# Kernel tuning notes

Measured on AMD Instinct MI355X. Metric: run time of the kernel, lower is better.

Reference implementation:

```python
import jax, jax.numpy as jnp
import numpy as np

B, S, HID = 2, 2048, 4096
H, KH, D = 32, 8, 128
WINDOW = 1024
THETA = 1000000.0


def setup_inputs() -> dict:
    key = jax.random.key(0)
    ks = jax.random.split(key, 5)
    scale = 0.02
    hidden_states = jax.random.normal(ks[0], (B, S, HID), dtype=jnp.float32)
    wq = jax.random.normal(ks[1], (HID, H * D), dtype=jnp.float32) * scale
    wk = jax.random.normal(ks[2], (HID, KH * D), dtype=jnp.float32) * scale
    wv = jax.random.normal(ks[3], (HID, KH * D), dtype=jnp.float32) * scale
    wo = jax.random.normal(ks[4], (H * D, HID), dtype=jnp.float32) * scale
    position_ids = jnp.broadcast_to(jnp.arange(S, dtype=jnp.int64 if jax.config.jax_enable_x64 else jnp.int32), (B, S))
    return {"hidden_states": hidden_states, "position_ids": position_ids,
            "wq": wq, "wk": wk, "wv": wv, "wo": wo}


def _rope_sin_cos(position_ids):
    # inv_freq over even dims, emb = concat(freqs, freqs) -> [b, s, D]
    inv_freq = 1.0 / (THETA ** (jnp.arange(0, D, 2, dtype=jnp.float32) / D))
    angles = position_ids.astype(jnp.float32)[..., None] * inv_freq  # [b, s, D/2]
    emb = jnp.concatenate([angles, angles], axis=-1)  # [b, s, D]
    return jnp.sin(emb)[:, None, :, :], jnp.cos(emb)[:, None, :, :]  # [b,1,s,D]


def _rotate_half(x):
    x1, x2 = jnp.split(x, 2, axis=-1)
    return jnp.concatenate([-x2, x1], axis=-1)


def _apply_rope(x, sin, cos):
    return x * cos + _rotate_half(x) * sin


def reference(hidden_states, position_ids, wq, wk, wv, wo):
    b, s, _ = hidden_states.shape
    # projections -> [b, heads, s, d]
    q = (hidden_states @ wq).reshape(b, s, H, D).transpose(0, 2, 1, 3)
    k = (hidden_states @ wk).reshape(b, s, KH, D).transpose(0, 2, 1, 3)
    v = (hidden_states @ wv).reshape(b, s, KH, D).transpose(0, 2, 1, 3)
    sin, cos = _rope_sin_cos(position_ids)
    q = _apply_rope(q, sin, cos)
    k = _apply_rope(k, sin, cos)
    # repeat kv heads for GQA: [b, KH, s, d] -> [b, H, s, d]
    rep = H // KH
    k = jnp.repeat(k, rep, axis=1)
    v = jnp.repeat(v, rep, axis=1)
    # sliding-window causal mask
    i = jnp.arange(s)[:, None]
    j = jnp.arange(s)[None, :]
    mask = (j <= i) & (i - j < WINDOW)  # [s, s]
    scores = jnp.einsum("bhqd,bhkd->bhqk", q, k) / jnp.sqrt(jnp.asarray(D, q.dtype))
    neg = jnp.finfo(scores.dtype).min
    scores = jnp.where(mask[None, None, :, :], scores, neg)
    attn = jax.nn.softmax(scores, axis=-1)
    out = jnp.einsum("bhqk,bhkd->bhqd", attn, v)
    out = out.transpose(0, 2, 1, 3).reshape(b, s, H * D)
    return out @ wo
```

## Files before the change

kernel.cpp:

```cpp
#include <hip/hip_runtime.h>
#include <hip/hip_bf16.h>
#include <math.h>

typedef __attribute__((ext_vector_type(8))) __bf16 bf16x8;
typedef __attribute__((ext_vector_type(4))) float f32x4;

#define MFMA16(a, b, c) __builtin_amdgcn_mfma_f32_16x16x32_bf16((a), (b), (c), 0, 0, 0)

__device__ inline void gld_lds16(const __hip_bfloat16* g, __hip_bfloat16* l) {
    __builtin_amdgcn_global_load_lds(
        (const __attribute__((address_space(1))) void*)g,
        (__attribute__((address_space(3))) void*)l, 16, 0, 0);
}

#define RAW_BARRIER() __builtin_amdgcn_s_barrier()
#define WAIT_LGKM0()                                          \
    do {                                                      \
        asm volatile("s_waitcnt lgkmcnt(0)" ::: "memory");    \
        __builtin_amdgcn_sched_barrier(0);                    \
    } while (0)
#define WAIT_VM(N) asm volatile("s_waitcnt vmcnt(" #N ")" ::: "memory")

__global__ void cast_bf16_kernel(const float* __restrict__ in, __hip_bfloat16* __restrict__ out) {
    int i = (blockIdx.x * blockDim.x + threadIdx.x) * 4;
    float4 v = *(const float4*)(in + i);
    out[i + 0] = __float2bfloat16(v.x);
    out[i + 1] = __float2bfloat16(v.y);
    out[i + 2] = __float2bfloat16(v.z);
    out[i + 3] = __float2bfloat16(v.w);
}

__global__ void transpose_cast_kernel(const float* __restrict__ w, __hip_bfloat16* __restrict__ wt,
                                      int K, int N) {
    __shared__ float tile[32][33];
    int n0 = blockIdx.x * 32, k0 = blockIdx.y * 32;
    int tx = threadIdx.x;
    int ty = threadIdx.y;
#pragma unroll
    for (int r = 0; r < 4; r++) {
        int k = k0 + ty + r * 8;
        tile[ty + r * 8][tx] = w[(size_t)k * N + n0 + tx];
    }
    __syncthreads();
#pragma unroll
    for (int r = 0; r < 4; r++) {
        int n = n0 + ty + r * 8;
        wt[(size_t)n * K + k0 + tx] = __float2bfloat16(tile[tx][ty + r * 8]);
    }
}

constexpr int TILE = 256 * 64;

template <typename EPILOGUE>
__device__ __forceinline__ void gemm256_8phase(
    const __hip_bfloat16* __restrict__ A, const __hip_bfloat16* __restrict__ Bt,
    int m0, int n0, int K, __hip_bfloat16* As, __hip_bfloat16* Bs, EPILOGUE epi) {
    int tid = threadIdx.x;
    int wave = tid >> 6, lane = tid & 63;
    int l15 = lane & 15, quad = lane >> 4;
    int wr = wave >> 2, wc = wave & 3;

    int lr = lane >> 3;
    int c8 = (lane & 7) ^ lr;
    const __hip_bfloat16* aG = A + (size_t)(m0 + wave * 8 + lr) * K + c8 * 8;
    const __hip_bfloat16* bG = Bt + (size_t)(n0 + wave * 8 + lr) * K + c8 * 8;
    int stRow = wave * 8;

    int e3 = l15 & 7;
    int s0 = (quad ^ e3) * 8;
    int s1 = ((4 + quad) ^ e3) * 8;

    f32x4 acc[8][4];
#pragma unroll
    for (int mi = 0; mi < 8; mi++)
#pragma unroll
        for (int ni = 0; ni < 4; ni++) acc[mi][ni] = (f32x4){0.f, 0.f, 0.f, 0.f};

    const int NT = K >> 6;

    auto stA = [&](int buf, int kt, int i) {
        gld_lds16(aG + (size_t)kt * 64 + (size_t)(i * 64) * K,
                  As + buf * TILE + (stRow + i * 64) * 64);
    };
    auto stB = [&](int buf, int kt, int i) {
        gld_lds16(bG + (size_t)kt * 64 + (size_t)(i * 64) * K,
                  Bs + buf * TILE + (stRow + i * 64) * 64);
    };

#pragma unroll
    for (int i = 0; i < 4; i++) stA(0, 0, i);
#pragma unroll
    for (int i = 0; i < 4; i++) stB(0, 0, i);
    {
        int k1 = (1 < NT) ? 1 : 0;
#pragma unroll
        for (int i = 0; i < 4; i++) stA(1, k1, i);
    }
    WAIT_VM(4);
    RAW_BARRIER();

    int cur = 0;
    for (int t = 0; t < NT; ++t) {
        int ktB = (t + 1 < NT) ? t + 1 : NT - 1;
        int ktA = (t + 2 < NT) ? t + 2 : NT - 1;
        const __hip_bfloat16* af = As + cur * TILE + (wr * 128 + l15) * 64;
        const __hip_bfloat16* bf = Bs + cur * TILE + (wc * 64 + l15) * 64;
        bf16x8 a0[4][2], a1[4][2], b0[2][2], b1[2][2];

#pragma unroll
        for (int mi = 0; mi < 4; mi++) {
            a0[mi][0] = *(const bf16x8*)(af + mi * 1024 + s0);
            a0[mi][1] = *(const bf16x8*)(af + mi * 1024 + s1);
        }
#pragma unroll
        for (int ni = 0; ni < 2; ni++) {
            b0[ni][0] = *(const bf16x8*)(bf + ni * 1024 + s0);
            b0[ni][1] = *(const bf16x8*)(bf + ni * 1024 + s1);
        }
        stB(cur ^ 1, ktB, 0);
        stB(cur ^ 1, ktB, 1);
        RAW_BARRIER();
        WAIT_LGKM0();
        __builtin_amdgcn_s_setprio(1);
#pragma unroll
        for (int mi = 0; mi < 4; mi++)
#pragma unroll
            for (int ni = 0; ni < 2; ni++) {
                acc[mi][ni] = MFMA16(a0[mi][0], b0[ni][0], acc[mi][ni]);
                acc[mi][ni] = MFMA16(a0[mi][1], b0[ni][1], acc[mi][ni]);
            }
        __builtin_amdgcn_s_setprio(0);
        RAW_BARRIER();

#pragma unroll
        for (int mi = 0; mi < 4; mi++) {
            a1[mi][0] = *(const bf16x8*)(af + (mi + 4) * 1024 + s0);
            a1[mi][1] = *(const bf16x8*)(af + (mi + 4) * 1024 + s1);
        }
        stB(cur ^ 1, ktB, 2);
        stB(cur ^ 1, ktB, 3);
        RAW_BARRIER();
        WAIT_LGKM0();
        __builtin_amdgcn_s_setprio(1);
#pragma unroll
        for (int mi = 0; mi < 4; mi++)
#pragma unroll
            for (int ni = 0; ni < 2; ni++) {
                acc[mi + 4][ni] = MFMA16(a1[mi][0], b0[ni][0], acc[mi + 4][ni]);
                acc[mi + 4][ni] = MFMA16(a1[mi][1], b0[ni][1], acc[mi + 4][ni]);
            }
        __builtin_amdgcn_s_setprio(0);
        RAW_BARRIER();

#pragma unroll
        for (int ni = 0; ni < 2; ni++) {
            b1[ni][0] = *(const bf16x8*)(bf + (ni + 2) * 1024 + s0);
            b1[ni][1] = *(const bf16x8*)(bf + (ni + 2) * 1024 + s1);
        }
        stA(cur, ktA, 0);
        stA(cur, ktA, 1);
        RAW_BARRIER();
        WAIT_LGKM0();
        __builtin_amdgcn_s_setprio(1);
#pragma unroll
        for (int mi = 0; mi < 4; mi++)
#pragma unroll
            for (int ni = 0; ni < 2; ni++) {
                acc[mi][ni + 2] = MFMA16(a0[mi][0], b1[ni][0], acc[mi][ni + 2]);
                acc[mi][ni + 2] = MFMA16(a0[mi][1], b1[ni][1], acc[mi][ni + 2]);
            }
        __builtin_amdgcn_s_setprio(0);
        RAW_BARRIER();

        stA(cur, ktA, 2);
        stA(cur, ktA, 3);
        RAW_BARRIER();
        __builtin_amdgcn_s_setprio(1);
#pragma unroll
        for (int mi = 0; mi < 4; mi++)
#pragma unroll
            for (int ni = 0; ni < 2; ni++) {
                acc[mi + 4][ni + 2] = MFMA16(a1[mi][0], b1[ni][0], acc[mi + 4][ni + 2]);
                acc[mi + 4][ni + 2] = MFMA16(a1[mi][1], b1[ni][1], acc[mi + 4][ni + 2]);
            }
        __builtin_amdgcn_s_setprio(0);
        WAIT_VM(4);
        RAW_BARRIER();
        cur ^= 1;
    }
    WAIT_VM(0);
    epi(acc, wr, wc, l15, quad);
}

__global__ __launch_bounds__(512, 2) void gemm_qkv_kernel(
    const __hip_bfloat16* __restrict__ Xb,
    const __hip_bfloat16* __restrict__ Wt,
    __hip_bfloat16* __restrict__ Qraw,
    __hip_bfloat16* __restrict__ Kraw,
    __hip_bfloat16* __restrict__ Vtt) {
    __shared__ __hip_bfloat16 As[2 * TILE];
    __shared__ __hip_bfloat16 Bs[2 * TILE];
    int m0 = blockIdx.y * 256, n0 = blockIdx.x * 256;
    gemm256_8phase(Xb, Wt, m0, n0, 4096, As, Bs,
        [&](f32x4 (&acc)[8][4], int wr, int wc, int l15, int quad) {
#pragma unroll
            for (int mi = 0; mi < 8; mi++) {
#pragma unroll
                for (int ni = 0; ni < 4; ni++) {
                    int n = n0 + wc * 64 + ni * 16 + l15;
#pragma unroll
                    for (int r = 0; r < 4; r++) {
                        int m = m0 + wr * 128 + mi * 16 + quad * 4 + r;
                        int bb = m >> 11, s = m & 2047;
                        __hip_bfloat16 hv = __float2bfloat16(acc[mi][ni][r]);
                        if (n < 4096) {
                            int hh = n >> 7, d = n & 127;
                            Qraw[(((size_t)(bb * 32 + hh)) * 2048 + s) * 128 + d] = hv;
                        } else if (n < 5120) {
                            int n2 = n - 4096, hh = n2 >> 7, d = n2 & 127;
                            Kraw[(((size_t)(bb * 8 + hh)) * 2048 + s) * 128 + d] = hv;
                        } else {
                            int n2 = n - 5120, hh = n2 >> 7, d = n2 & 127;
                            Vtt[((((size_t)(bb * 8 + hh)) * 32 + (s >> 6)) * 128 + d) * 64 + (s & 63)] = hv;
                        }
                    }
                }
            }
        });
}

__global__ __launch_bounds__(512, 2) void gemm_out_kernel(
    const __hip_bfloat16* __restrict__ A, const __hip_bfloat16* __restrict__ Bt,
    float* __restrict__ C) {
    __shared__ __hip_bfloat16 As[2 * TILE];
    __shared__ __hip_bfloat16 Bs[2 * TILE];
    int m0 = blockIdx.y * 256, n0 = blockIdx.x * 256;
    gemm256_8phase(A, Bt, m0, n0, 4096, As, Bs,
        [&](f32x4 (&acc)[8][4], int wr, int wc, int l15, int quad) {
            const int N = 4096;
#pragma unroll
            for (int mi = 0; mi < 8; mi++) {
#pragma unroll
                for (int ni = 0; ni < 4; ni++) {
                    int n = n0 + wc * 64 + ni * 16 + l15;
#pragma unroll
                    for (int r = 0; r < 4; r++) {
                        int m = m0 + wr * 128 + mi * 16 + quad * 4 + r;
                        C[(size_t)m * N + n] = acc[mi][ni][r];
                    }
                }
            }
        });
}

__global__ void rope_kernel(__hip_bfloat16* __restrict__ x, const int* __restrict__ pos_ids,
                            int nheads) {
    int idx = blockIdx.x * blockDim.x + threadIdx.x;
    int d = idx & 63;
    int s = (idx >> 6) & 2047;
    int bh = idx >> 17;
    int b = bh / nheads;
    float p = (float)pos_ids[b * 2048 + s];
    float inv = exp2f(-(float)d * 0.31143075889f);
    float ang = p * inv;
    float sn, cs;
    __sincosf(ang, &sn, &cs);
    size_t base = ((size_t)bh * 2048 + s) * 128;
    float x1 = __bfloat162float(x[base + d]);
    float x2 = __bfloat162float(x[base + d + 64]);
    x[base + d]      = __float2bfloat16(x1 * cs - x2 * sn);
    x[base + d + 64] = __float2bfloat16(x2 * cs + x1 * sn);
}

__global__ __launch_bounds__(256) void attn_kernel(
    const __hip_bfloat16* __restrict__ Qb, const __hip_bfloat16* __restrict__ Kb,
    const __hip_bfloat16* __restrict__ Vtt, __hip_bfloat16* __restrict__ AO) {
    const int S = 2048, D = 128;
    __shared__ __hip_bfloat16 Ks[64 * 128];
    __shared__ __hip_bfloat16 Vs[128 * 64];
    __shared__ __hip_bfloat16 Pl[4][16][72];

    int tid = threadIdx.x;
    int wave = tid >> 6, lane = tid & 63;
    int l15 = lane & 15, quad = lane >> 4;
    int base = blockIdx.x * 64;
    int i0 = base + wave * 16;
    int h = blockIdx.y, b = blockIdx.z;
    int kh = h >> 2;
    const __hip_bfloat16* Qh = Qb + (size_t)(b * 32 + h) * S * D;
    const __hip_bfloat16* Kh = Kb + (size_t)(b * 8 + kh) * S * D;
    const __hip_bfloat16* Vh = Vtt + (size_t)(b * 8 + kh) * S * D;

    bf16x8 qf[4];
    {
        const __hip_bfloat16* qrow = Qh + (size_t)(i0 + l15) * D + quad * 8;
#pragma unroll
        for (int kk = 0; kk < 4; kk++) qf[kk] = *(const bf16x8*)(qrow + kk * 32);
    }
    f32x4 o[8];
#pragma unroll
    for (int f = 0; f < 8; f++) o[f] = (f32x4){0.f, 0.f, 0.f, 0.f};
    float lrow[4] = {0.f, 0.f, 0.f, 0.f};

    int kst = (base > 1023) ? ((base - 1023) & ~63) : 0;
    const float c2 = 0.12751878882f;
    int e3 = l15 & 7;

    for (int key0 = kst; key0 <= base; key0 += 64) {
#pragma unroll
        for (int i = 0; i < 4; i++) {
            int rb = wave * 16 + i * 4;
            int row = rb + (lane >> 4);
            int c = (lane & 15) ^ (row & 7);
            gld_lds16(Kh + (size_t)(key0 + row) * 128 + c * 8, Ks + rb * 128);
        }
        const __hip_bfloat16* Vtile = Vh + (size_t)(key0 >> 6) * (128 * 64);
#pragma unroll
        for (int i = 0; i < 4; i++) {
            int db = wave * 32 + i * 8;
            int row = db + (lane >> 3);
            int c = (lane & 7) ^ (row & 7);
            gld_lds16(Vtile + (size_t)row * 64 + c * 8, Vs + db * 64);
        }
        __syncthreads();

        bool alive = (key0 <= i0 + 15) && (key0 + 63 >= i0 - 1023);
        if (alive) {
            f32x4 sc[4];
#pragma unroll
            for (int kb = 0; kb < 4; kb++) {
                sc[kb] = (f32x4){0.f, 0.f, 0.f, 0.f};
                const __hip_bfloat16* krow = Ks + (kb * 16 + l15) * 128;
#pragma unroll
                for (int kk = 0; kk < 4; kk++) {
                    int slot = ((kk << 2) | quad) ^ e3;
                    bf16x8 kf = *(const bf16x8*)(krow + slot * 8);
                    sc[kb] = MFMA16(qf[kk], kf, sc[kb]);
                }
            }
            bool interior = (key0 + 63 <= i0) && (key0 >= i0 - 1008);
            if (interior) {
#pragma unroll
                for (int kb = 0; kb < 4; kb++)
#pragma unroll
                    for (int r = 0; r < 4; r++) {
                        float p = __builtin_amdgcn_exp2f(sc[kb][r] * c2);
                        lrow[r] += p;
                        Pl[wave][quad * 4 + r][kb * 16 + l15] = __float2bfloat16(p);
                    }
            } else {
#pragma unroll
                for (int kb = 0; kb < 4; kb++)
#pragma unroll
                    for (int r = 0; r < 4; r++) {
                        int i = i0 + quad * 4 + r;
                        int j = key0 + kb * 16 + l15;
                        float v = (j <= i && i - j < 1024) ? sc[kb][r] * c2 : -1e30f;
                        float p = __builtin_amdgcn_exp2f(v);
                        lrow[r] += p;
                        Pl[wave][quad * 4 + r][kb * 16 + l15] = __float2bfloat16(p);
                    }
            }
            bf16x8 pf0 = *(const bf16x8*)(&Pl[wave][l15][quad * 8]);
            bf16x8 pf1 = *(const bf16x8*)(&Pl[wave][l15][32 + quad * 8]);
            int s0 = quad ^ e3, s1 = (4 + quad) ^ e3;
#pragma unroll
            for (int f = 0; f < 8; f++) {
                const __hip_bfloat16* vrow = Vs + (f * 16 + l15) * 64;
                bf16x8 v0 = *(const bf16x8*)(vrow + s0 * 8);
                bf16x8 v1 = *(const bf16x8*)(vrow + s1 * 8);
                o[f] = MFMA16(pf0, v0, o[f]);
                o[f] = MFMA16(pf1, v1, o[f]);
            }
        }
        __syncthreads();
    }

#pragma unroll
    for (int r = 0; r < 4; r++) {
#pragma unroll
        for (int msk = 1; msk < 16; msk <<= 1) lrow[r] += __shfl_xor(lrow[r], msk, 64);
    }
#pragma unroll
    for (int r = 0; r < 4; r++) {
        int srow = i0 + quad * 4 + r;
        float invl = 1.f / lrow[r];
        __hip_bfloat16* orow = AO + ((size_t)(b * 2048 + srow) * 4096) + h * 128;
#pragma unroll
        for (int f = 0; f < 8; f++) orow[f * 16 + l15] = __float2bfloat16(o[f][r] * invl);
    }
}

extern "C" void kernel_launch(void* const* d_in, const int* in_sizes, int n_in,
                              void* d_out, int out_size, void* d_ws, size_t ws_size,
                              hipStream_t stream) {
    (void)in_sizes; (void)n_in; (void)out_size;
    const float* hidden = (const float*)d_in[0];
    const int* pos = (const int*)d_in[1];
    const float* wq = (const float*)d_in[2];
    const float* wk = (const float*)d_in[3];
    const float* wv = (const float*)d_in[4];
    const float* wo = (const float*)d_in[5];
    float* out = (float*)d_out;

    const int M = 4096;
    char* ws = (char*)d_ws;
    size_t off = 0;
    auto alloc = [&](size_t bytes) { char* p = ws + off; off += bytes; return p; };
    __hip_bfloat16* Xb    = (__hip_bfloat16*)alloc((size_t)M * 4096 * 2);
    __hip_bfloat16* Wqkvt = (__hip_bfloat16*)alloc((size_t)6144 * 4096 * 2);
    __hip_bfloat16* Wot   = (__hip_bfloat16*)alloc((size_t)4096 * 4096 * 2);
    __hip_bfloat16* Qb    = (__hip_bfloat16*)alloc((size_t)M * 4096 * 2);
    __hip_bfloat16* Kb    = (__hip_bfloat16*)alloc((size_t)M * 1024 * 2);
    __hip_bfloat16* Vtt   = (__hip_bfloat16*)alloc((size_t)M * 1024 * 2);
    __hip_bfloat16* AO    = (__hip_bfloat16*)alloc((size_t)M * 4096 * 2);
    if (off > ws_size) return;

    cast_bf16_kernel<<<(M * 4096) / 1024, 256, 0, stream>>>(hidden, Xb);
    dim3 tb(32, 8);
    transpose_cast_kernel<<<dim3(128, 128), tb, 0, stream>>>(wq, Wqkvt, 4096, 4096);
    transpose_cast_kernel<<<dim3(32, 128),  tb, 0, stream>>>(wk, Wqkvt + (size_t)4096 * 4096, 4096, 1024);
    transpose_cast_kernel<<<dim3(32, 128),  tb, 0, stream>>>(wv, Wqkvt + (size_t)5120 * 4096, 4096, 1024);
    transpose_cast_kernel<<<dim3(128, 128), tb, 0, stream>>>(wo, Wot, 4096, 4096);

    gemm_qkv_kernel<<<dim3(24, 16), 512, 0, stream>>>(Xb, Wqkvt, Qb, Kb, Vtt);

    rope_kernel<<<(2 * 32 * 2048 * 64) / 256, 256, 0, stream>>>(Qb, pos, 32);
    rope_kernel<<<(2 * 8 * 2048 * 64) / 256, 256, 0, stream>>>(Kb, pos, 8);

    attn_kernel<<<dim3(32, 32, 2), 256, 0, stream>>>(Qb, Kb, Vtt, AO);

    gemm_out_kernel<<<dim3(16, 16), 512, 0, stream>>>(AO, Wot, out);
}
```

Before: 841.6 us.

## Double-buffer attention K/V tiles and use smaller-tile QKV GEMM

```diff
diff --git a/kernel.cpp b/kernel.cpp
--- a/kernel.cpp
+++ b/kernel.cpp
@@ -49,168 +49,83 @@
     }
 }
 
-constexpr int TILE = 256 * 64;
-
 template <typename EPILOGUE>
-__device__ __forceinline__ void gemm256_8phase(
+__device__ __forceinline__ void gemm128_bk64(
     const __hip_bfloat16* __restrict__ A, const __hip_bfloat16* __restrict__ Bt,
     int m0, int n0, int K, __hip_bfloat16* As, __hip_bfloat16* Bs, EPILOGUE epi) {
     int tid = threadIdx.x;
     int wave = tid >> 6, lane = tid & 63;
     int l15 = lane & 15, quad = lane >> 4;
-    int wr = wave >> 2, wc = wave & 3;
 
     int lr = lane >> 3;
     int c8 = (lane & 7) ^ lr;
     const __hip_bfloat16* aG = A + (size_t)(m0 + wave * 8 + lr) * K + c8 * 8;
     const __hip_bfloat16* bG = Bt + (size_t)(n0 + wave * 8 + lr) * K + c8 * 8;
-    int stRow = wave * 8;
-
+    __hip_bfloat16* aL = As + wave * 512;
+    __hip_bfloat16* bL = Bs + wave * 512;
+
+    int wm = wave & 1, wn = wave >> 1;
     int e3 = l15 & 7;
     int s0 = (quad ^ e3) * 8;
     int s1 = ((4 + quad) ^ e3) * 8;
-
-    f32x4 acc[8][4];
-#pragma unroll
-    for (int mi = 0; mi < 8; mi++)
+    const __hip_bfloat16* afr = As + (wm * 64 + l15) * 64;
+    const __hip_bfloat16* bfr = Bs + (wn * 64 + l15) * 64;
+
+    f32x4 acc[4][4];
+#pragma unroll
+    for (int mi = 0; mi < 4; mi++)
 #pragma unroll
         for (int ni = 0; ni < 4; ni++) acc[mi][ni] = (f32x4){0.f, 0.f, 0.f, 0.f};
 
-    const int NT = K >> 6;
-
-    auto stA = [&](int buf, int kt, int i) {
-        gld_lds16(aG + (size_t)kt * 64 + (size_t)(i * 64) * K,
-                  As + buf * TILE + (stRow + i * 64) * 64);
-    };
-    auto stB = [&](int buf, int kt, int i) {
-        gld_lds16(bG + (size_t)kt * 64 + (size_t)(i * 64) * K,
-                  Bs + buf * TILE + (stRow + i * 64) * 64);
-    };
-
-#pragma unroll
-    for (int i = 0; i < 4; i++) stA(0, 0, i);
-#pragma unroll
-    for (int i = 0; i < 4; i++) stB(0, 0, i);
-    {
-        int k1 = (1 < NT) ? 1 : 0;
-#pragma unroll
-        for (int i = 0; i < 4; i++) stA(1, k1, i);
-    }
-    WAIT_VM(4);
-    RAW_BARRIER();
-
-    int cur = 0;
-    for (int t = 0; t < NT; ++t) {
-        int ktB = (t + 1 < NT) ? t + 1 : NT - 1;
-        int ktA = (t + 2 < NT) ? t + 2 : NT - 1;
-        const __hip_bfloat16* af = As + cur * TILE + (wr * 128 + l15) * 64;
-        const __hip_bfloat16* bf = Bs + cur * TILE + (wc * 64 + l15) * 64;
-        bf16x8 a0[4][2], a1[4][2], b0[2][2], b1[2][2];
-
+    for (int k0 = 0; k0 < K; k0 += 64) {
+#pragma unroll
+        for (int i = 0; i < 4; i++) {
+            gld_lds16(aG + k0 + (size_t)(i * 32) * K, aL + i * 2048);
+            gld_lds16(bG + k0 + (size_t)(i * 32) * K, bL + i * 2048);
+        }
+        __syncthreads();
+        bf16x8 a0[4], b0[4], a1[4], b1[4];
 #pragma unroll
         for (int mi = 0; mi < 4; mi++) {
-            a0[mi][0] = *(const bf16x8*)(af + mi * 1024 + s0);
-            a0[mi][1] = *(const bf16x8*)(af + mi * 1024 + s1);
-        }
-#pragma unroll
-        for (int ni = 0; ni < 2; ni++) {
-            b0[ni][0] = *(const bf16x8*)(bf + ni * 1024 + s0);
-            b0[ni][1] = *(const bf16x8*)(bf + ni * 1024 + s1);
-        }
-        stB(cur ^ 1, ktB, 0);
-        stB(cur ^ 1, ktB, 1);
-        RAW_BARRIER();
-        WAIT_LGKM0();
-        __builtin_amdgcn_s_setprio(1);
+            a0[mi] = *(const bf16x8*)(afr + mi * 1024 + s0);
+            a1[mi] = *(const bf16x8*)(afr + mi * 1024 + s1);
+        }
+#pragma unroll
+        for (int ni = 0; ni < 4; ni++) {
+            b0[ni] = *(const bf16x8*)(bfr + ni * 1024 + s0);
+            b1[ni] = *(const bf16x8*)(bfr + ni * 1024 + s1);
+        }
 #pragma unroll
         for (int mi = 0; mi < 4; mi++)
 #pragma unroll
-            for (int ni = 0; ni < 2; ni++) {
-                acc[mi][ni] = MFMA16(a0[mi][0], b0[ni][0], acc[mi][ni]);
-                acc[mi][ni] = MFMA16(a0[mi][1], b0[ni][1], acc[mi][ni]);
-            }
-        __builtin_amdgcn_s_setprio(0);
-        RAW_BARRIER();
-
-#pragma unroll
-        for (int mi = 0; mi < 4; mi++) {
-            a1[mi][0] = *(const bf16x8*)(af + (mi + 4) * 1024 + s0);
-            a1[mi][1] = *(const bf16x8*)(af + (mi + 4) * 1024 + s1);
-        }
-        stB(cur ^ 1, ktB, 2);
-        stB(cur ^ 1, ktB, 3);
-        RAW_BARRIER();
-        WAIT_LGKM0();
-        __builtin_amdgcn_s_setprio(1);
-#pragma unroll
-        for (int mi = 0; mi < 4; mi++)
-#pragma unroll
-            for (int ni = 0; ni < 2; ni++) {
-                acc[mi + 4][ni] = MFMA16(a1[mi][0], b0[ni][0], acc[mi + 4][ni]);
-                acc[mi + 4][ni] = MFMA16(a1[mi][1], b0[ni][1], acc[mi + 4][ni]);
-            }
-        __builtin_amdgcn_s_setprio(0);
-        RAW_BARRIER();
-
-#pragma unroll
-        for (int ni = 0; ni < 2; ni++) {
-            b1[ni][0] = *(const bf16x8*)(bf + (ni + 2) * 1024 + s0);
-            b1[ni][1] = *(const bf16x8*)(bf + (ni + 2) * 1024 + s1);
-        }
-        stA(cur, ktA, 0);
-        stA(cur, ktA, 1);
-        RAW_BARRIER();
-        WAIT_LGKM0();
-        __builtin_amdgcn_s_setprio(1);
-#pragma unroll
-        for (int mi = 0; mi < 4; mi++)
-#pragma unroll
-            for (int ni = 0; ni < 2; ni++) {
-                acc[mi][ni + 2] = MFMA16(a0[mi][0], b1[ni][0], acc[mi][ni + 2]);
-                acc[mi][ni + 2] = MFMA16(a0[mi][1], b1[ni][1], acc[mi][ni + 2]);
-            }
-        __builtin_amdgcn_s_setprio(0);
-        RAW_BARRIER();
-
-        stA(cur, ktA, 2);
-        stA(cur, ktA, 3);
-        RAW_BARRIER();
-        __builtin_amdgcn_s_setprio(1);
-#pragma unroll
-        for (int mi = 0; mi < 4; mi++)
-#pragma unroll
-            for (int ni = 0; ni < 2; ni++) {
-                acc[mi + 4][ni + 2] = MFMA16(a1[mi][0], b1[ni][0], acc[mi + 4][ni + 2]);
-                acc[mi + 4][ni + 2] = MFMA16(a1[mi][1], b1[ni][1], acc[mi + 4][ni + 2]);
-            }
-        __builtin_amdgcn_s_setprio(0);
-        WAIT_VM(4);
-        RAW_BARRIER();
-        cur ^= 1;
-    }
-    WAIT_VM(0);
-    epi(acc, wr, wc, l15, quad);
-}
-
-__global__ __launch_bounds__(512, 2) void gemm_qkv_kernel(
+            for (int ni = 0; ni < 4; ni++) {
+                acc[mi][ni] = MFMA16(a0[mi], b0[ni], acc[mi][ni]);
+                acc[mi][ni] = MFMA16(a1[mi], b1[ni], acc[mi][ni]);
+            }
+        __syncthreads();
+    }
+    epi(acc, wm, wn, l15, quad);
+}
+
+__global__ __launch_bounds__(256) void gemm_qkv_kernel(
     const __hip_bfloat16* __restrict__ Xb,
     const __hip_bfloat16* __restrict__ Wt,
     __hip_bfloat16* __restrict__ Qraw,
     __hip_bfloat16* __restrict__ Kraw,
     __hip_bfloat16* __restrict__ Vtt) {
-    __shared__ __hip_bfloat16 As[2 * TILE];
-    __shared__ __hip_bfloat16 Bs[2 * TILE];
-    int m0 = blockIdx.y * 256, n0 = blockIdx.x * 256;
-    gemm256_8phase(Xb, Wt, m0, n0, 4096, As, Bs,
-        [&](f32x4 (&acc)[8][4], int wr, int wc, int l15, int quad) {
-#pragma unroll
-            for (int mi = 0; mi < 8; mi++) {
+    __shared__ __hip_bfloat16 As[128 * 64];
+    __shared__ __hip_bfloat16 Bs[128 * 64];
+    int m0 = blockIdx.y * 128, n0 = blockIdx.x * 128;
+    gemm128_bk64(Xb, Wt, m0, n0, 4096, As, Bs,
+        [&](f32x4 (&acc)[4][4], int wm, int wn, int l15, int quad) {
+#pragma unroll
+            for (int mi = 0; mi < 4; mi++) {
 #pragma unroll
                 for (int ni = 0; ni < 4; ni++) {
-                    int n = n0 + wc * 64 + ni * 16 + l15;
+                    int n = n0 + wn * 64 + ni * 16 + l15;
 #pragma unroll
                     for (int r = 0; r < 4; r++) {
-                        int m = m0 + wr * 128 + mi * 16 + quad * 4 + r;
+                        int m = m0 + wm * 64 + mi * 16 + quad * 4 + r;
                         int bb = m >> 11, s = m & 2047;
                         __hip_bfloat16 hv = __float2bfloat16(acc[mi][ni][r]);
                         if (n < 4096) {
@@ -227,6 +142,149 @@
                 }
             }
         });
+}
+
+constexpr int TILE = 256 * 64;
+
+template <typename EPILOGUE>
+__device__ __forceinline__ void gemm256_8phase(
+    const __hip_bfloat16* __restrict__ A, const __hip_bfloat16* __restrict__ Bt,
+    int m0, int n0, int K, __hip_bfloat16* As, __hip_bfloat16* Bs, EPILOGUE epi) {
+    int tid = threadIdx.x;
+    int wave = tid >> 6, lane = tid & 63;
+    int l15 = lane & 15, quad = lane >> 4;
+    int wr = wave >> 2, wc = wave & 3;
+
+    int lr = lane >> 3;
+    int c8 = (lane & 7) ^ lr;
+    const __hip_bfloat16* aG = A + (size_t)(m0 + wave * 8 + lr) * K + c8 * 8;
+    const __hip_bfloat16* bG = Bt + (size_t)(n0 + wave * 8 + lr) * K + c8 * 8;
+    int stRow = wave * 8;
+
+    int e3 = l15 & 7;
+    int s0 = (quad ^ e3) * 8;
+    int s1 = ((4 + quad) ^ e3) * 8;
+
+    f32x4 acc[8][4];
+#pragma unroll
+    for (int mi = 0; mi < 8; mi++)
+#pragma unroll
+        for (int ni = 0; ni < 4; ni++) acc[mi][ni] = (f32x4){0.f, 0.f, 0.f, 0.f};
+
+    const int NT = K >> 6;
+
+    auto stA = [&](int buf, int kt, int i) {
+        gld_lds16(aG + (size_t)kt * 64 + (size_t)(i * 64) * K,
+                  As + buf * TILE + (stRow + i * 64) * 64);
+    };
+    auto stB = [&](int buf, int kt, int i) {
+        gld_lds16(bG + (size_t)kt * 64 + (size_t)(i * 64) * K,
+                  Bs + buf * TILE + (stRow + i * 64) * 64);
+    };
+
+#pragma unroll
+    for (int i = 0; i < 4; i++) stA(0, 0, i);
+#pragma unroll
+    for (int i = 0; i < 4; i++) stB(0, 0, i);
+    {
+        int k1 = (1 < NT) ? 1 : 0;
+#pragma unroll
+        for (int i = 0; i < 4; i++) stA(1, k1, i);
+    }
+    WAIT_VM(4);
+    RAW_BARRIER();
+
+    int cur = 0;
+    for (int t = 0; t < NT; ++t) {
+        int ktB = (t + 1 < NT) ? t + 1 : NT - 1;
+        int ktA = (t + 2 < NT) ? t + 2 : NT - 1;
+        const __hip_bfloat16* af = As + cur * TILE + (wr * 128 + l15) * 64;
+        const __hip_bfloat16* bf = Bs + cur * TILE + (wc * 64 + l15) * 64;
+        bf16x8 a0[4][2], a1[4][2], b0[2][2], b1[2][2];
+
+#pragma unroll
+        for (int mi = 0; mi < 4; mi++) {
+            a0[mi][0] = *(const bf16x8*)(af + mi * 1024 + s0);
+            a0[mi][1] = *(const bf16x8*)(af + mi * 1024 + s1);
+        }
+#pragma unroll
+        for (int ni = 0; ni < 2; ni++) {
+            b0[ni][0] = *(const bf16x8*)(bf + ni * 1024 + s0);
+            b0[ni][1] = *(const bf16x8*)(bf + ni * 1024 + s1);
+        }
+        stB(cur ^ 1, ktB, 0);
+        stB(cur ^ 1, ktB, 1);
+        RAW_BARRIER();
+        WAIT_LGKM0();
+        __builtin_amdgcn_s_setprio(1);
+#pragma unroll
+        for (int mi = 0; mi < 4; mi++)
+#pragma unroll
+            for (int ni = 0; ni < 2; ni++) {
+                acc[mi][ni] = MFMA16(a0[mi][0], b0[ni][0], acc[mi][ni]);
+                acc[mi][ni] = MFMA16(a0[mi][1], b0[ni][1], acc[mi][ni]);
+            }
+        __builtin_amdgcn_s_setprio(0);
+        RAW_BARRIER();
+
+#pragma unroll
+        for (int mi = 0; mi < 4; mi++) {
+            a1[mi][0] = *(const bf16x8*)(af + (mi + 4) * 1024 + s0);
+            a1[mi][1] = *(const bf16x8*)(af + (mi + 4) * 1024 + s1);
+        }
+        stB(cur ^ 1, ktB, 2);
+        stB(cur ^ 1, ktB, 3);
+        RAW_BARRIER();
+        WAIT_LGKM0();
+        __builtin_amdgcn_s_setprio(1);
+#pragma unroll
+        for (int mi = 0; mi < 4; mi++)
+#pragma unroll
+            for (int ni = 0; ni < 2; ni++) {
+                acc[mi + 4][ni] = MFMA16(a1[mi][0], b0[ni][0], acc[mi + 4][ni]);
+                acc[mi + 4][ni] = MFMA16(a1[mi][1], b0[ni][1], acc[mi + 4][ni]);
+            }
+        __builtin_amdgcn_s_setprio(0);
+        RAW_BARRIER();
+
+#pragma unroll
+        for (int ni = 0; ni < 2; ni++) {
+            b1[ni][0] = *(const bf16x8*)(bf + (ni + 2) * 1024 + s0);
+            b1[ni][1] = *(const bf16x8*)(bf + (ni + 2) * 1024 + s1);
+        }
+        stA(cur, ktA, 0);
+        stA(cur, ktA, 1);
+        RAW_BARRIER();
+        WAIT_LGKM0();
+        __builtin_amdgcn_s_setprio(1);
+#pragma unroll
+        for (int mi = 0; mi < 4; mi++)
+#pragma unroll
+            for (int ni = 0; ni < 2; ni++) {
+                acc[mi][ni + 2] = MFMA16(a0[mi][0], b1[ni][0], acc[mi][ni + 2]);
+                acc[mi][ni + 2] = MFMA16(a0[mi][1], b1[ni][1], acc[mi][ni + 2]);
+            }
+        __builtin_amdgcn_s_setprio(0);
+        RAW_BARRIER();
+
+        stA(cur, ktA, 2);
+        stA(cur, ktA, 3);
+        RAW_BARRIER();
+        __builtin_amdgcn_s_setprio(1);
+#pragma unroll
+        for (int mi = 0; mi < 4; mi++)
+#pragma unroll
+            for (int ni = 0; ni < 2; ni++) {
+                acc[mi + 4][ni + 2] = MFMA16(a1[mi][0], b1[ni][0], acc[mi + 4][ni + 2]);
+                acc[mi + 4][ni + 2] = MFMA16(a1[mi][1], b1[ni][1], acc[mi + 4][ni + 2]);
+            }
+        __builtin_amdgcn_s_setprio(0);
+        WAIT_VM(4);
+        RAW_BARRIER();
+        cur ^= 1;
+    }
+    WAIT_VM(0);
+    epi(acc, wr, wc, l15, quad);
 }
 
 __global__ __launch_bounds__(512, 2) void gemm_out_kernel(
@@ -276,8 +334,8 @@
     const __hip_bfloat16* __restrict__ Qb, const __hip_bfloat16* __restrict__ Kb,
     const __hip_bfloat16* __restrict__ Vtt, __hip_bfloat16* __restrict__ AO) {
     const int S = 2048, D = 128;
-    __shared__ __hip_bfloat16 Ks[64 * 128];
-    __shared__ __hip_bfloat16 Vs[128 * 64];
+    __shared__ __hip_bfloat16 Ks[2][64 * 128];
+    __shared__ __hip_bfloat16 Vs[2][128 * 64];
     __shared__ __hip_bfloat16 Pl[4][16][72];
 
     int tid = threadIdx.x;
@@ -306,13 +364,13 @@
     const float c2 = 0.12751878882f;
     int e3 = l15 & 7;
 
-    for (int key0 = kst; key0 <= base; key0 += 64) {
+    auto stage = [&](int key0, int buf) {
 #pragma unroll
         for (int i = 0; i < 4; i++) {
             int rb = wave * 16 + i * 4;
             int row = rb + (lane >> 4);
             int c = (lane & 15) ^ (row & 7);
-            gld_lds16(Kh + (size_t)(key0 + row) * 128 + c * 8, Ks + rb * 128);
+            gld_lds16(Kh + (size_t)(key0 + row) * 128 + c * 8, &Ks[buf][rb * 128]);
         }
         const __hip_bfloat16* Vtile = Vh + (size_t)(key0 >> 6) * (128 * 64);
 #pragma unroll
@@ -320,17 +378,30 @@
             int db = wave * 32 + i * 8;
             int row = db + (lane >> 3);
             int c = (lane & 7) ^ (row & 7);
-            gld_lds16(Vtile + (size_t)row * 64 + c * 8, Vs + db * 64);
-        }
-        __syncthreads();
+            gld_lds16(Vtile + (size_t)row * 64 + c * 8, &Vs[buf][db * 64]);
+        }
+    };
+
+    stage(kst, 0);
+
+    for (int key0 = kst; key0 <= base; key0 += 64) {
+        int buf = ((key0 - kst) >> 6) & 1;
+        if (key0 + 64 <= base) {
+            stage(key0 + 64, buf ^ 1);
+            WAIT_VM(8);
+        } else {
+            WAIT_VM(0);
+        }
+        RAW_BARRIER();
 
         bool alive = (key0 <= i0 + 15) && (key0 + 63 >= i0 - 1023);
         if (alive) {
             f32x4 sc[4];
+            __builtin_amdgcn_s_setprio(1);
 #pragma unroll
             for (int kb = 0; kb < 4; kb++) {
                 sc[kb] = (f32x4){0.f, 0.f, 0.f, 0.f};
-                const __hip_bfloat16* krow = Ks + (kb * 16 + l15) * 128;
+                const __hip_bfloat16* krow = &Ks[buf][(kb * 16 + l15) * 128];
 #pragma unroll
                 for (int kk = 0; kk < 4; kk++) {
                     int slot = ((kk << 2) | quad) ^ e3;
@@ -338,6 +409,7 @@
                     sc[kb] = MFMA16(qf[kk], kf, sc[kb]);
                 }
             }
+            __builtin_amdgcn_s_setprio(0);
             bool interior = (key0 + 63 <= i0) && (key0 >= i0 - 1008);
             if (interior) {
 #pragma unroll
@@ -364,16 +436,18 @@
             bf16x8 pf0 = *(const bf16x8*)(&Pl[wave][l15][quad * 8]);
             bf16x8 pf1 = *(const bf16x8*)(&Pl[wave][l15][32 + quad * 8]);
             int s0 = quad ^ e3, s1 = (4 + quad) ^ e3;
+            __builtin_amdgcn_s_setprio(1);
 #pragma unroll
             for (int f = 0; f < 8; f++) {
-                const __hip_bfloat16* vrow = Vs + (f * 16 + l15) * 64;
+                const __hip_bfloat16* vrow = &Vs[buf][(f * 16 + l15) * 64];
                 bf16x8 v0 = *(const bf16x8*)(vrow + s0 * 8);
                 bf16x8 v1 = *(const bf16x8*)(vrow + s1 * 8);
                 o[f] = MFMA16(pf0, v0, o[f]);
                 o[f] = MFMA16(pf1, v1, o[f]);
             }
-        }
-        __syncthreads();
+            __builtin_amdgcn_s_setprio(0);
+        }
+        RAW_BARRIER();
     }
 
 #pragma unroll
@@ -423,7 +497,7 @@
     transpose_cast_kernel<<<dim3(32, 128),  tb, 0, stream>>>(wv, Wqkvt + (size_t)5120 * 4096, 4096, 1024);
     transpose_cast_kernel<<<dim3(128, 128), tb, 0, stream>>>(wo, Wot, 4096, 4096);
 
-    gemm_qkv_kernel<<<dim3(24, 16), 512, 0, stream>>>(Xb, Wqkvt, Qb, Kb, Vtt);
+    gemm_qkv_kernel<<<dim3(48, 32), 256, 0, stream>>>(Xb, Wqkvt, Qb, Kb, Vtt);
 
     rope_kernel<<<(2 * 32 * 2048 * 64) / 256, 256, 0, stream>>>(Qb, pos, 32);
     rope_kernel<<<(2 * 8 * 2048 * 64) / 256, 256, 0, stream>>>(Kb, pos, 8);
```

Measured after the change: 809.6 us. 1.04x faster.
